# Kernel optimization log

Measured on AMD Instinct MI355X. Metric: run time of the kernel, lower is better.

The kernel has to match this reference:

```python
import jax, jax.numpy as jnp
import numpy as np
from jax import lax

D = 256          # embed_dims
NLP = 2          # NumLinePoints
B, H, W = 4, 64, 64
NQ = H * W       # 4096
NK = 4096
BN_EPS = 0.001


def setup_inputs() -> dict:
    key = jax.random.key(0)
    ks = jax.random.split(key, 16)
    inp = {
        "query": jax.random.normal(ks[0], (B, D, H, W), jnp.float32),
        "v": jax.random.normal(ks[1], (B, NK, D), jnp.float32),
        "query_pos": jax.random.normal(ks[2], (B, NQ, D), jnp.float32),
        "key_pos": jax.random.normal(ks[3], (B, NK, D), jnp.float32),
        "other_W": jax.random.uniform(ks[4], (B, NK), jnp.float32),
        # params (torch Linear convention: weight [out, in], y = x @ W.T + b)
        "w_vs": jax.random.normal(ks[5], (D, D), jnp.float32) * (1.0 / np.sqrt(D)),
        "mlp_w1": jax.random.normal(ks[6], (D, 2 * D), jnp.float32) * (1.0 / np.sqrt(2 * D)),
        "mlp_b1": jnp.zeros((D,), jnp.float32),
        "mlp_w2": jax.random.normal(ks[7], (D, D), jnp.float32) * (1.0 / np.sqrt(D)),
        "mlp_b2": jnp.zeros((D,), jnp.float32),
        "conv1_w": jax.random.normal(ks[8], (D, D, 3, 3), jnp.float32) * (1.0 / np.sqrt(9 * D)),
        "bn_gamma": jnp.ones((D,), jnp.float32),
        "bn_beta": jnp.zeros((D,), jnp.float32),
        "bn_mean": jnp.zeros((D,), jnp.float32),
        "bn_var": jnp.ones((D,), jnp.float32),
        "conv2_w": jax.random.normal(ks[9], (D, D, 1, 1), jnp.float32) * (1.0 / np.sqrt(D)),
        "conv2_b": jnp.zeros((D,), jnp.float32),
    }
    return inp


def _forward(query, v, query_pos, key_pos, other_W,
             w_vs, mlp_w1, mlp_b1, mlp_w2, mlp_b2,
             conv1_w, bn_gamma, bn_beta, bn_mean, bn_var,
             conv2_w, conv2_b):
    # v projection (no bias)
    v = jnp.einsum('bkd,ed->bke', v, w_vs)
    # ref_point_head: repeat query_pos along feature dim, then 2-layer MLP
    qp = jnp.concatenate([query_pos] * NLP, axis=-1)          # [B,NQ,2D]
    qp = jax.nn.relu(jnp.einsum('bqd,hd->bqh', qp, mlp_w1) + mlp_b1)
    qp = jnp.einsum('bqh,eh->bqe', qp, mlp_w2) + mlp_b2       # [B,NQ,D]
    # L2 normalize
    qn = qp / jnp.linalg.norm(qp, axis=-1, keepdims=True)
    kn = key_pos / jnp.linalg.norm(key_pos, axis=-1, keepdims=True)
    # similarity + ReLU + elementwise mask
    rel = jax.nn.relu(jnp.einsum('bqd,bkd->bqk', qn, kn))     # [B,NQ,NK]
    rel = rel * other_W[:, None, :]
    out = jnp.einsum('bqk,bkd->bqd', rel, v)                  # [B,NQ,D]
    # reshape to feature map [B,D,H,W]
    out = out.transpose(0, 2, 1).reshape(query.shape)
    # fuse: conv3x3 (no bias) + BN (eval) + SiLU, then conv1x1 (+bias)
    x = lax.conv_general_dilated(out, conv1_w, (1, 1), 'SAME',
                                 dimension_numbers=('NCHW', 'OIHW', 'NCHW'))
    inv = bn_gamma / jnp.sqrt(bn_var + BN_EPS)
    x = x * inv[None, :, None, None] + (bn_beta - bn_mean * inv)[None, :, None, None]
    x = x * jax.nn.sigmoid(x)  # SiLU
    x = lax.conv_general_dilated(x, conv2_w, (1, 1), 'SAME',
                                 dimension_numbers=('NCHW', 'OIHW', 'NCHW'))
    x = x + conv2_b[None, :, None, None]
    return query + x


def reference(query, v, query_pos, key_pos, other_W,
              w_vs, mlp_w1, mlp_b1, mlp_w2, mlp_b2,
              conv1_w, bn_gamma, bn_beta, bn_mean, bn_var,
              conv2_w, conv2_b):
    return _forward(query, v, query_pos, key_pos, other_W,
                    w_vs, mlp_w1, mlp_b1, mlp_w2, mlp_b2,
                    conv1_w, bn_gamma, bn_beta, bn_mean, bn_var,
                    conv2_w, conv2_b)
```

## Files before the change

kernel.cpp:

```cpp
#include <hip/hip_runtime.h>
#include <math.h>

constexpr int kB  = 4;
constexpr int kD  = 256;
constexpr int kNQ = 4096;
constexpr int kNK = 4096;
constexpr int kHW = 4096;

typedef __bf16 bf16x8 __attribute__((ext_vector_type(8)));
typedef float  f32x16 __attribute__((ext_vector_type(16)));

__device__ __forceinline__ unsigned short f2bf(float x) {
    unsigned int u = __builtin_bit_cast(unsigned int, x);
    u = (u + 0x7fffu + ((u >> 16) & 1u)) >> 16;
    return (unsigned short)u;
}

__global__ __launch_bounds__(256) void k_prep(
    const float* __restrict__ v_in, const float* __restrict__ ow, ushort* __restrict__ v_bf,
    const float* __restrict__ qpos, ushort* __restrict__ qpos_bf,
    const float* __restrict__ kpos, ushort* __restrict__ kn_bf,
    const float* __restrict__ conv1_w, ushort* __restrict__ w9p,
    const float* __restrict__ w_vs, ushort* __restrict__ wvs_bf,
    const float* __restrict__ mlp_w2, ushort* __restrict__ w2_bf,
    const float* __restrict__ conv2_w, ushort* __restrict__ c2_bf,
    const float* __restrict__ mlp_w1, ushort* __restrict__ w1e_bf)
{
    const int bid = blockIdx.x, t = threadIdx.x;
    if (bid < 4096) {
        const int i = bid * 256 + t;
        float4 v = ((const float4*)v_in)[i];
        const float wsc = ow[i >> 6];
        ushort4 o;
        o.x = f2bf(v.x * wsc); o.y = f2bf(v.y * wsc);
        o.z = f2bf(v.z * wsc); o.w = f2bf(v.w * wsc);
        ((ushort4*)v_bf)[i] = o;
    } else if (bid < 8192) {
        const int i = (bid - 4096) * 256 + t;
        float4 v = ((const float4*)qpos)[i];
        ushort4 o;
        o.x = f2bf(v.x); o.y = f2bf(v.y); o.z = f2bf(v.z); o.w = f2bf(v.w);
        ((ushort4*)qpos_bf)[i] = o;
    } else if (bid < 12288) {
        const int row  = (bid - 8192) * 4 + (t >> 6);
        const int lane = t & 63;
        float4 v = ((const float4*)(kpos + (size_t)row * 256))[lane];
        float ss = v.x * v.x + v.y * v.y + v.z * v.z + v.w * v.w;
        #pragma unroll
        for (int off = 32; off; off >>= 1) ss += __shfl_xor(ss, off, 64);
        const float rn = 1.0f / sqrtf(ss);
        ushort4 o;
        o.x = f2bf(v.x * rn); o.y = f2bf(v.y * rn);
        o.z = f2bf(v.z * rn); o.w = f2bf(v.w * rn);
        ((ushort4*)(kn_bf + (size_t)row * 256))[lane] = o;
    } else if (bid < 14592) {
        const int idx = bid - 12288;
        const int s = idx >> 8, co = idx & 255, ci = t;
        const int oidx = ((s * 8 + (co >> 5)) * 16 + (ci >> 4)) * 512
                       + ((ci >> 3) & 1) * 256 + (co & 31) * 8 + (ci & 7);
        w9p[oidx] = f2bf(conv1_w[((size_t)co * 256 + ci) * 9 + s]);
    } else if (bid < 14784) {
        const float* src = (bid < 14656) ? w_vs : (bid < 14720) ? mlp_w2 : conv2_w;
        ushort* dst = (bid < 14656) ? wvs_bf : (bid < 14720) ? w2_bf : c2_bf;
        const int i = ((bid - 14592) & 63) * 256 + t;
        float4 v = ((const float4*)src)[i];
        ushort4 o;
        o.x = f2bf(v.x); o.y = f2bf(v.y); o.z = f2bf(v.z); o.w = f2bf(v.w);
        ((ushort4*)dst)[i] = o;
    } else {
        const int h = bid - 14784;
        w1e_bf[h * 256 + t] = f2bf(mlp_w1[h * 512 + t] + mlp_w1[h * 512 + 256 + t]);
    }
}

template<int EPI, int RELU>
__global__ __launch_bounds__(256, 2) void k_gemm_mfma(
    const ushort* __restrict__ A, const ushort* __restrict__ W,
    const float* __restrict__ bias, void* __restrict__ outp)
{
    const int t = threadIdx.x, w = t >> 6, l = t & 63, lr = l & 31, lh = l >> 5;
    const int m0 = (blockIdx.x >> 2) * 128;
    const int n0 = (blockIdx.x & 3) * 64;
    const int wm = w >> 1, wn = w & 1;
    const ushort* Ar0 = A + (size_t)(m0 + wm * 64 + lr) * 256 + lh * 8;
    const ushort* Ar1 = Ar0 + 32 * 256;
    const ushort* Wr  = W + (size_t)(n0 + wn * 32 + lr) * 256 + lh * 8;
    f32x16 c0{}, c1{};
    #pragma unroll
    for (int ks = 0; ks < 16; ++ks) {
        bf16x8 a0 = *(const bf16x8*)(Ar0 + ks * 16);
        bf16x8 a1 = *(const bf16x8*)(Ar1 + ks * 16);
        bf16x8 wf = *(const bf16x8*)(Wr + ks * 16);
        c0 = __builtin_amdgcn_mfma_f32_32x32x16_bf16(a0, wf, c0, 0, 0, 0);
        c1 = __builtin_amdgcn_mfma_f32_32x32x16_bf16(a1, wf, c1, 0, 0, 0);
    }
    const int n = n0 + wn * 32 + lr;
    float bb = bias ? bias[n] : 0.f;
    if constexpr (EPI == 2) {
        __shared__ ushort tr[64][136];
        #pragma unroll
        for (int r = 0; r < 16; ++r) {
            const int ml = wm * 64 + (r & 3) + 8 * (r >> 2) + 4 * lh;
            float v0 = c0[r], v1 = c1[r];
            if (RELU) { v0 = fmaxf(v0, 0.f); v1 = fmaxf(v1, 0.f); }
            tr[wn * 32 + lr][ml]      = f2bf(v0);
            tr[wn * 32 + lr][ml + 32] = f2bf(v1);
        }
        __syncthreads();
        ushort* out = (ushort*)outp;
        const int b = m0 >> 12, mm = m0 & 4095;
        const int row = t >> 2, seg = t & 3;
        uint4 u0 = *(uint4*)&tr[row][seg * 32];
        uint4 u1 = *(uint4*)&tr[row][seg * 32 + 8];
        uint4 u2 = *(uint4*)&tr[row][seg * 32 + 16];
        uint4 u3 = *(uint4*)&tr[row][seg * 32 + 24];
        ushort* ob = out + ((size_t)(b * 128 + (mm >> 5) + seg) * 256 + n0 + row) * 32;
        *(uint4*)ob        = u0; *(uint4*)(ob + 8)  = u1;
        *(uint4*)(ob + 16) = u2; *(uint4*)(ob + 24) = u3;
    } else {
        #pragma unroll
        for (int r = 0; r < 16; ++r) {
            const int m = m0 + wm * 64 + (r & 3) + 8 * (r >> 2) + 4 * lh;
            float v0 = c0[r] + bb, v1 = c1[r] + bb;
            if (RELU) { v0 = fmaxf(v0, 0.f); v1 = fmaxf(v1, 0.f); }
            if constexpr (EPI == 0) {
                float* out = (float*)outp;
                out[(size_t)m * 256 + n]      = v0;
                out[(size_t)(m + 32) * 256 + n] = v1;
            } else {
                ushort* out = (ushort*)outp;
                out[(size_t)m * 256 + n]      = f2bf(v0);
                out[(size_t)(m + 32) * 256 + n] = f2bf(v1);
            }
        }
    }
}

__global__ __launch_bounds__(256) void k_l2norm_bf16(const float* __restrict__ in,
                                                     ushort* __restrict__ out) {
    const int row  = blockIdx.x * 4 + (threadIdx.x >> 6);
    const int lane = threadIdx.x & 63;
    float4 v = ((const float4*)(in + (size_t)row * 256))[lane];
    float ss = v.x * v.x + v.y * v.y + v.z * v.z + v.w * v.w;
    #pragma unroll
    for (int off = 32; off; off >>= 1) ss += __shfl_xor(ss, off, 64);
    const float rn = 1.0f / sqrtf(ss);
    ushort4 o;
    o.x = f2bf(v.x * rn); o.y = f2bf(v.y * rn);
    o.z = f2bf(v.z * rn); o.w = f2bf(v.w * rn);
    ((ushort4*)(out + (size_t)row * 256))[lane] = o;
}

__global__ __launch_bounds__(512, 2) void k_attn_mfma(
    const ushort* __restrict__ qn, const ushort* __restrict__ kn,
    const ushort* __restrict__ vpT, ushort* __restrict__ X)
{
    __shared__ __align__(16) char lds[147456];
    const int t = threadIdx.x, w = t >> 6, l = t & 63, lr = l & 31, lh = l >> 5;
    const int dh = w >> 2, qg = (w >> 1) & 1, kh = w & 1;
    const int bid0 = blockIdx.x;
    const int L = (bid0 & 7) * 32 + (bid0 >> 3);
    const int b = L >> 6, qt = L & 63;
    const int q0 = qt << 6;
    union U4 { unsigned u[4]; bf16x8 v; };

    int koff[4], voff[4];
    #pragma unroll
    for (int i = 0; i < 4; ++i) {
        const int p = i * 512 + t;
        {
            const int R = p >> 5, sl = p & 31;
            koff[i] = R * 512 + ((sl ^ (R & 31)) << 4);
        }
        {
            const int sub = p >> 10, q = p & 1023;
            const int R = q >> 4, ch = (q & 15) ^ (R & 15);
            voff[i] = sub * 16384 + ((ch >> 2) * 64 + R) * 64 + ((ch & 3) << 4);
        }
    }
    const char* kgb = (const char*)(kn + (size_t)b * 4096 * 256);
    const char* vgb = (const char*)vpT + (size_t)b * 128 * 16384;

    #define STAGE_K(bb, tc) do { \
        const char* ks_ = kgb + (size_t)(tc) * 32768; \
        char* kd_ = lds + (bb) * 32768; \
        _Pragma("unroll") \
        for (int i_ = 0; i_ < 4; ++i_) \
            __builtin_amdgcn_global_load_lds( \
                (const __attribute__((address_space(1))) unsigned*)(ks_ + koff[i_]), \
                (__attribute__((address_space(3))) unsigned*)(kd_ + (i_ * 512 + w * 64) * 16), 16, 0, 0); \
        } while (0)
    #define STAGE_V(bb, tc) do { \
        const char* vs_ = vgb + (size_t)(tc) * 32768; \
        char* vd_ = lds + 65536 + (bb) * 32768; \
        _Pragma("unroll") \
        for (int i_ = 0; i_ < 4; ++i_) \
            __builtin_amdgcn_global_load_lds( \
                (const __attribute__((address_space(1))) unsigned*)(vs_ + voff[i_]), \
                (__attribute__((address_space(3))) unsigned*)(vd_ + (i_ * 512 + w * 64) * 16), 16, 0, 0); \
        } while (0)

    const ushort* qrow = qn + ((size_t)b * 4096 + q0 + qg * 32 + lr) * 256 + lh * 8;
    bf16x8 qf[16];
    #pragma unroll
    for (int ks = 0; ks < 16; ++ks) qf[ks] = *(const bf16x8*)(qrow + ks * 16);

    f32x16 oa0{}, oa1{}, oa2{}, oa3{};
    bf16x8 pf0{}, pf1{};

    STAGE_K(0, 0);
    __syncthreads();
    for (int tt = 0; tt <= 64; ++tt) {
        if (tt < 64) {
            if (tt + 1 < 64) STAGE_K((tt + 1) & 1, tt + 1);
            STAGE_V(tt & 1, tt);
        }
        if (tt > 0) {
            const char* vb = lds + 65536 + ((tt - 1) & 1) * 32768 + kh * 16384;
            bf16x8 qp0, qp1;
            if (dh == 0) { qp0 = pf0; qp1 = pf1; }
            else {
                const unsigned* pr = (const unsigned*)(lds + 131072
                                   + ((tt - 1) & 1) * 8192 + (qg * 2 + kh) * 2048);
                U4 a0, a1;
                #pragma unroll
                for (int wd = 0; wd < 4; ++wd) {
                    a0.u[wd] = pr[wd * 64 + l];
                    a1.u[wd] = pr[(4 + wd) * 64 + l];
                }
                qp0 = a0.v; qp1 = a1.v;
            }
            #define PVD(OA, DB) { \
                const int R_  = (((DB) & 1)) * 32 + lr; \
                const int sg_ = dh * 2 + ((DB) >> 1); \
                bf16x8 v0_ = *(const bf16x8*)(vb + R_ * 256 + ((((sg_ << 2) + lh)     ^ (lr & 15)) << 4)); \
                bf16x8 v1_ = *(const bf16x8*)(vb + R_ * 256 + ((((sg_ << 2) + 2 + lh) ^ (lr & 15)) << 4)); \
                OA = __builtin_amdgcn_mfma_f32_32x32x16_bf16(v0_, qp0, OA, 0, 0, 0); \
                OA = __builtin_amdgcn_mfma_f32_32x32x16_bf16(v1_, qp1, OA, 0, 0, 0); }
            PVD(oa0, 0) PVD(oa1, 1) PVD(oa2, 2) PVD(oa3, 3)
            #undef PVD
        }
        if (dh == 0 && tt < 64) {
            const char* kb = lds + (tt & 1) * 32768 + kh * 16384;
            f32x16 s0{}, s1{}, s2{}, s3{};
            #pragma unroll
            for (int ks = 0; ks < 16; ks += 4) {
                bf16x8 k0 = *(const bf16x8*)(kb + lr * 512 + (((2 * ks     + lh) ^ lr) << 4));
                bf16x8 k1 = *(const bf16x8*)(kb + lr * 512 + (((2 * ks + 2 + lh) ^ lr) << 4));
                bf16x8 k2 = *(const bf16x8*)(kb + lr * 512 + (((2 * ks + 4 + lh) ^ lr) << 4));
                bf16x8 k3 = *(const bf16x8*)(kb + lr * 512 + (((2 * ks + 6 + lh) ^ lr) << 4));
                s0 = __builtin_amdgcn_mfma_f32_32x32x16_bf16(k0, qf[ks],     s0, 0, 0, 0);
                s1 = __builtin_amdgcn_mfma_f32_32x32x16_bf16(k1, qf[ks + 1], s1, 0, 0, 0);
                s2 = __builtin_amdgcn_mfma_f32_32x32x16_bf16(k2, qf[ks + 2], s2, 0, 0, 0);
                s3 = __builtin_amdgcn_mfma_f32_32x32x16_bf16(k3, qf[ks + 3], s3, 0, 0, 0);
            }
            f32x16 s = (s0 + s1) + (s2 + s3);
            #define PKR(A, B) ((unsigned)f2bf(fmaxf((A), 0.f)) | ((unsigned)f2bf(fmaxf((B), 0.f)) << 16))
            unsigned p01 = PKR(s[0],  s[1]),  p23 = PKR(s[2],  s[3]);
            unsigned p45 = PKR(s[4],  s[5]),  p67 = PKR(s[6],  s[7]);
            unsigned p89 = PKR(s[8],  s[9]),  pAB = PKR(s[10], s[11]);
            unsigned pCD = PKR(s[12], s[13]), pEF = PKR(s[14], s[15]);
            #undef PKR
            unsigned e1a = lh ? p01 : p45,  e2a = lh ? p23 : p67;
            unsigned e1b = lh ? p89 : pCD,  e2b = lh ? pAB : pEF;
            unsigned f1a = (unsigned)__shfl_xor((int)e1a, 32, 64);
            unsigned f2a = (unsigned)__shfl_xor((int)e2a, 32, 64);
            unsigned f1b = (unsigned)__shfl_xor((int)e1b, 32, 64);
            unsigned f2b = (unsigned)__shfl_xor((int)e2b, 32, 64);
            U4 a0, a1;
            a0.u[0] = lh ? f1a : p01;  a0.u[1] = lh ? f2a : p23;
            a0.u[2] = lh ? p45 : f1a;  a0.u[3] = lh ? p67 : f2a;
            a1.u[0] = lh ? f1b : p89;  a1.u[1] = lh ? f2b : pAB;
            a1.u[2] = lh ? pCD : f1b;  a1.u[3] = lh ? pEF : f2b;
            pf0 = a0.v; pf1 = a1.v;
            unsigned* pw = (unsigned*)(lds + 131072 + (tt & 1) * 8192 + (qg * 2 + kh) * 2048);
            #pragma unroll
            for (int wd = 0; wd < 4; ++wd) {
                pw[wd * 64 + l]       = a0.u[wd];
                pw[(4 + wd) * 64 + l] = a1.u[wd];
            }
        }
        if (tt < 64) __syncthreads();
    }
    #undef STAGE_K
    #undef STAGE_V
    float* red = (float*)lds;
    const int rowbase = ((qg * 2 + dh) * 32 + lr) * 132;
    if (kh == 1) {
        #define REDW(OA, DB) _Pragma("unroll") \
            for (int r = 0; r < 16; r += 2) { \
                const int d_ = (DB) * 32 + (r & 3) + 8 * (r >> 2) + 4 * lh; \
                *(float2*)&red[rowbase + d_] = make_float2((OA)[r], (OA)[r + 1]); }
        REDW(oa0, 0) REDW(oa1, 1) REDW(oa2, 2) REDW(oa3, 3)
        #undef REDW
    }
    __syncthreads();
    if (kh == 0) {
        ushort* Xb = X + ((size_t)b * 4096 + q0 + qg * 32 + lr) * 256 + dh * 128;
        #define OUTD(OA, DB) _Pragma("unroll") \
            for (int r = 0; r < 16; r += 2) { \
                const int d_ = (DB) * 32 + (r & 3) + 8 * (r >> 2) + 4 * lh; \
                float2 p = *(float2*)&red[rowbase + d_]; \
                ushort2 u_; u_.x = f2bf((OA)[r] + p.x); u_.y = f2bf((OA)[r + 1] + p.y); \
                *(ushort2*)(Xb + d_) = u_; }
        OUTD(oa0, 0) OUTD(oa1, 1) OUTD(oa2, 2) OUTD(oa3, 3)
        #undef OUTD
    }
}

__global__ __launch_bounds__(256, 2) void k_conv3_mfma(
    const ushort* __restrict__ X, const ushort* __restrict__ w9p,
    const float* __restrict__ bn_g, const float* __restrict__ bn_b,
    const float* __restrict__ bn_m, const float* __restrict__ bn_v,
    ushort* __restrict__ Y)
{
    __shared__ __align__(16) char smem[67584];
    float* bnv = (float*)(smem + 65536);
    const int t = threadIdx.x, w = t >> 6, l = t & 63, lr = l & 31, lh = l >> 5;
    {
        float inv = bn_g[t] * rsqrtf(bn_v[t] + 1e-3f);
        bnv[t]       = inv;
        bnv[256 + t] = bn_b[t] - bn_m[t] * inv;
    }
    const int bid = blockIdx.x;
    const int b = bid >> 7, ct = (bid >> 5) & 3, pt = bid & 31;
    const int co0 = ct * 64, p0 = pt * 128;
    const int wc = w >> 1, wp = w & 1;
    const int h0 = pt * 2 + wp;
    const int cb = ct * 2 + wc;
    const char* Xbytes = (const char*)(X + (size_t)b * 4096 * 256);
    const bf16x8 bz = {};
    f32x16 o0{}, o1{};

    #define CSTAGE(bufb, st_) do { \
        const char* src_ = Xbytes + (ptrdiff_t)(p0 + 64 * ((st_) >> 1) - 64) * 512 \
                         + ((st_) & 1) * 256; \
        char* dst_ = smem + (bufb) * 32768; \
        _Pragma("unroll") \
        for (int i_ = 0; i_ < 8; ++i_) { \
            const int di_ = i_ * 256 + t; \
            const int R_ = di_ >> 4, sl_ = di_ & 15; \
            __builtin_amdgcn_global_load_lds( \
                (const __attribute__((address_space(1))) unsigned*)(src_ + (ptrdiff_t)R_ * 512 + ((sl_ ^ (R_ & 15)) << 4)), \
                (__attribute__((address_space(3))) unsigned*)(dst_ + di_ * 16), 16, 0, 0); \
        } } while (0)

    CSTAGE(0, 0);
    __syncthreads();
    for (int st = 0; st < 6; ++st) {
        if (st < 5) CSTAGE((st + 1) & 1, st + 1);
        if (st < 5) asm volatile("s_waitcnt vmcnt(8)" ::: "memory");
        else        asm volatile("s_waitcnt vmcnt(0)" ::: "memory");
        __builtin_amdgcn_s_barrier();
        const char* xb = smem + (st & 1) * 32768;
        const int dyi = st >> 1, cih = st & 1;
        const int hh = h0 + dyi - 1;
        if (hh >= 0 && hh <= 63) {
            __builtin_amdgcn_s_setprio(1);
            #pragma unroll
            for (int dxi = 0; dxi < 3; ++dxi) {
                const int dx = dxi - 1;
                const int s = dyi * 3 + dxi;
                const bool mA = (dxi == 0) && (lr == 0);
                const bool mB = (dxi == 2) && (lr == 31);
                const int R0 = mA ? 0 : (wp * 64 + lr + dx);
                const int R1 = mB ? 0 : (wp * 64 + lr + dx + 32);
                const ushort* wb = w9p + ((size_t)(s * 8 + cb) * 16 + cih * 8) * 512 + l * 8;
                #pragma unroll
                for (int k8 = 0; k8 < 8; ++k8) {
                    bf16x8 af = *(const bf16x8*)(wb + k8 * 512);
                    bf16x8 b0 = *(const bf16x8*)(xb + R0 * 256 + (((k8 * 2 + lh) ^ (R0 & 15)) << 4));
                    bf16x8 b1 = *(const bf16x8*)(xb + R1 * 256 + (((k8 * 2 + lh) ^ (R1 & 15)) << 4));
                    if (mA) b0 = bz;
                    if (mB) b1 = bz;
                    o0 = __builtin_amdgcn_mfma_f32_32x32x16_bf16(af, b0, o0, 0, 0, 0);
                    o1 = __builtin_amdgcn_mfma_f32_32x32x16_bf16(af, b1, o1, 0, 0, 0);
                }
            }
            __builtin_amdgcn_s_setprio(0);
        }
        __builtin_amdgcn_s_barrier();
    }
    #undef CSTAGE
    ushort (*tr)[72] = (ushort(*)[72])smem;
    #pragma unroll
    for (int r = 0; r < 16; ++r) {
        const int co_l = wc * 32 + (r & 3) + 8 * (r >> 2) + 4 * lh;
        const int co = co0 + co_l;
        const float inv = bnv[co], add = bnv[256 + co];
        float x0 = o0[r] * inv + add;
        float x1 = o1[r] * inv + add;
        x0 = x0 / (1.f + expf(-x0));
        x1 = x1 / (1.f + expf(-x1));
        tr[wp * 64 + lr][co_l]      = f2bf(x0);
        tr[wp * 64 + 32 + lr][co_l] = f2bf(x1);
    }
    __syncthreads();
    const int pp = t >> 1, half = t & 1;
    uint4 u0 = *(uint4*)&tr[pp][half * 32];
    uint4 u1 = *(uint4*)&tr[pp][half * 32 + 8];
    uint4 u2 = *(uint4*)&tr[pp][half * 32 + 16];
    uint4 u3 = *(uint4*)&tr[pp][half * 32 + 24];
    ushort* yb = Y + ((size_t)b * 4096 + p0 + pp) * 256 + co0 + half * 32;
    *(uint4*)yb        = u0; *(uint4*)(yb + 8)  = u1;
    *(uint4*)(yb + 16) = u2; *(uint4*)(yb + 24) = u3;
}

__global__ __launch_bounds__(256, 2) void k_conv1x1_mfma(
    const ushort* __restrict__ Y, const ushort* __restrict__ W2,
    const float* __restrict__ bias2, const float* __restrict__ query,
    float* __restrict__ out)
{
    const int t = threadIdx.x, w = t >> 6, l = t & 63, lr = l & 31, lh = l >> 5;
    const int bid = blockIdx.x;
    const int b = bid >> 7, ct = (bid >> 5) & 3, pt = bid & 31;
    const int co0 = ct * 64, p0 = pt * 128;
    const int wc = w >> 1, wp = w & 1;
    const ushort* Wr = W2 + (size_t)(co0 + wc * 32 + lr) * 256 + lh * 8;
    const ushort* Yp = Y + ((size_t)b * 4096 + p0 + wp * 64 + lr) * 256 + lh * 8;
    f32x16 o0{}, o1{};
    #pragma unroll
    for (int ks = 0; ks < 16; ++ks) {
        bf16x8 wf = *(const bf16x8*)(Wr + ks * 16);
        bf16x8 y0 = *(const bf16x8*)(Yp + ks * 16);
        bf16x8 y1 = *(const bf16x8*)(Yp + 32 * 256 + ks * 16);
        o0 = __builtin_amdgcn_mfma_f32_32x32x16_bf16(wf, y0, o0, 0, 0, 0);
        o1 = __builtin_amdgcn_mfma_f32_32x32x16_bf16(wf, y1, o1, 0, 0, 0);
    }
    #pragma unroll
    for (int r = 0; r < 16; ++r) {
        const int co = co0 + wc * 32 + (r & 3) + 8 * (r >> 2) + 4 * lh;
        const float bb = bias2[co];
        const size_t base = ((size_t)b * 256 + co) * 4096 + p0 + wp * 64 + lr;
        out[base]      = o0[r] + bb + query[base];
        out[base + 32] = o1[r] + bb + query[base + 32];
    }
}

extern "C" void kernel_launch(void* const* d_in, const int* in_sizes, int n_in,
                              void* d_out, int out_size, void* d_ws, size_t ws_size,
                              hipStream_t stream) {
    const float* query   = (const float*)d_in[0];
    const float* v_in    = (const float*)d_in[1];
    const float* qpos    = (const float*)d_in[2];
    const float* kpos    = (const float*)d_in[3];
    const float* otherW  = (const float*)d_in[4];
    const float* w_vs    = (const float*)d_in[5];
    const float* mlp_w1  = (const float*)d_in[6];
    const float* mlp_b1  = (const float*)d_in[7];
    const float* mlp_w2  = (const float*)d_in[8];
    const float* mlp_b2  = (const float*)d_in[9];
    const float* conv1_w = (const float*)d_in[10];
    const float* bn_g    = (const float*)d_in[11];
    const float* bn_b    = (const float*)d_in[12];
    const float* bn_m    = (const float*)d_in[13];
    const float* bn_v    = (const float*)d_in[14];
    const float* conv2_w = (const float*)d_in[15];
    const float* conv2_b = (const float*)d_in[16];
    float* out = (float*)d_out;
    char* base = (char*)d_ws;

    constexpr size_t MB = 1u << 20;
    ushort* v_bf    = (ushort*)(base);
    ushort* qpos_bf = (ushort*)(base + 8 * MB);
    float*  qp_f32  = (float*) (base);
    ushort* qhid_bf = (ushort*)(base + 16 * MB);
    ushort* X_bf    = (ushort*)(base + 16 * MB);
    ushort* qn_bf   = (ushort*)(base + 24 * MB);
    ushort* Y_bf    = (ushort*)(base + 24 * MB);
    ushort* kn_bf   = (ushort*)(base + 32 * MB);
    ushort* vT_bf   = (ushort*)(base + 40 * MB);
    ushort* wvs_bf  = (ushort*)(base + 48 * MB);
    ushort* w1e_bf  = (ushort*)(base + 48 * MB + 128 * 1024);
    ushort* w2_bf   = (ushort*)(base + 48 * MB + 256 * 1024);
    ushort* c2_bf   = (ushort*)(base + 48 * MB + 384 * 1024);
    ushort* w9p_bf  = (ushort*)(base + 48 * MB + 512 * 1024);

    k_prep<<<15040, 256, 0, stream>>>(v_in, otherW, v_bf, qpos, qpos_bf,
                                      kpos, kn_bf, conv1_w, w9p_bf,
                                      w_vs, wvs_bf, mlp_w2, w2_bf,
                                      conv2_w, c2_bf, mlp_w1, w1e_bf);
    k_gemm_mfma<2, 0><<<512, 256, 0, stream>>>(v_bf, wvs_bf, nullptr, vT_bf);
    k_gemm_mfma<1, 1><<<512, 256, 0, stream>>>(qpos_bf, w1e_bf, mlp_b1, qhid_bf);
    k_gemm_mfma<0, 0><<<512, 256, 0, stream>>>(qhid_bf, w2_bf, mlp_b2, qp_f32);
    k_l2norm_bf16<<<4096, 256, 0, stream>>>(qp_f32, qn_bf);
    k_attn_mfma<<<256, 512, 0, stream>>>(qn_bf, kn_bf, vT_bf, X_bf);
    k_conv3_mfma<<<512, 256, 0, stream>>>(X_bf, w9p_bf, bn_g, bn_b, bn_m, bn_v, Y_bf);
    k_conv1x1_mfma<<<512, 256, 0, stream>>>(Y_bf, c2_bf, conv2_b, query, out);
}
```

Baseline: 209.4 us.

## Stage GEMM and 1x1-conv tiles in swizzled LDS with 128x128 blocks

The projection/MLP GEMMs and the final 1x1 conv move from 128x64 tiles, where each wave read its operands straight from global memory, to 128x128 tiles per 512-thread block. Both operand tiles are first copied into 128KB of LDS with direct global-to-LDS loads, using an XOR swizzle so the MFMA fragment reads avoid bank conflicts. This is meant to cut redundant global traffic, since operands are now shared across eight waves. In exchange it allows one block per CU, halves the grid, and has no overlap between the bulk load and compute.

```diff
diff --git a/kernel.cpp b/kernel.cpp
--- a/kernel.cpp
+++ b/kernel.cpp
@@ -74,30 +74,49 @@
 }
 
 template<int EPI, int RELU>
-__global__ __launch_bounds__(256, 2) void k_gemm_mfma(
+__global__ __launch_bounds__(512, 1) void k_gemm_mfma(
     const ushort* __restrict__ A, const ushort* __restrict__ W,
     const float* __restrict__ bias, void* __restrict__ outp)
 {
+    __shared__ __align__(16) char lds[131072];
     const int t = threadIdx.x, w = t >> 6, l = t & 63, lr = l & 31, lh = l >> 5;
-    const int m0 = (blockIdx.x >> 2) * 128;
-    const int n0 = (blockIdx.x & 3) * 64;
-    const int wm = w >> 1, wn = w & 1;
-    const ushort* Ar0 = A + (size_t)(m0 + wm * 64 + lr) * 256 + lh * 8;
-    const ushort* Ar1 = Ar0 + 32 * 256;
-    const ushort* Wr  = W + (size_t)(n0 + wn * 32 + lr) * 256 + lh * 8;
+    const int wm = w >> 2, wn = w & 3;
+    const int m0 = (blockIdx.x >> 1) * 128;
+    const int n0 = (blockIdx.x & 1) * 128;
+    const char* Ab = (const char*)A + (size_t)m0 * 512;
+    const char* Wb = (const char*)W + (size_t)n0 * 512;
+    #pragma unroll
+    for (int i = 0; i < 8; ++i) {
+        const int p = i * 512 + t;
+        const int R = p >> 5, sl = p & 31;
+        const int so = R * 512 + ((sl ^ (R & 31)) << 4);
+        __builtin_amdgcn_global_load_lds(
+            (const __attribute__((address_space(1))) unsigned*)(Ab + so),
+            (__attribute__((address_space(3))) unsigned*)(lds + p * 16), 16, 0, 0);
+        __builtin_amdgcn_global_load_lds(
+            (const __attribute__((address_space(1))) unsigned*)(Wb + so),
+            (__attribute__((address_space(3))) unsigned*)(lds + 65536 + p * 16), 16, 0, 0);
+    }
+    __syncthreads();
+    const char* Abuf = lds;
+    const char* Wbuf = lds + 65536;
+    const int ar0 = wm * 64 + lr, ar1 = ar0 + 32;
+    const int wrr = wn * 32 + lr;
     f32x16 c0{}, c1{};
     #pragma unroll
     for (int ks = 0; ks < 16; ++ks) {
-        bf16x8 a0 = *(const bf16x8*)(Ar0 + ks * 16);
-        bf16x8 a1 = *(const bf16x8*)(Ar1 + ks * 16);
-        bf16x8 wf = *(const bf16x8*)(Wr + ks * 16);
+        const int j = 2 * ks + lh;
+        bf16x8 a0 = *(const bf16x8*)(Abuf + ar0 * 512 + ((j ^ lr) << 4));
+        bf16x8 a1 = *(const bf16x8*)(Abuf + ar1 * 512 + ((j ^ lr) << 4));
+        bf16x8 wf = *(const bf16x8*)(Wbuf + wrr * 512 + ((j ^ lr) << 4));
         c0 = __builtin_amdgcn_mfma_f32_32x32x16_bf16(a0, wf, c0, 0, 0, 0);
         c1 = __builtin_amdgcn_mfma_f32_32x32x16_bf16(a1, wf, c1, 0, 0, 0);
     }
     const int n = n0 + wn * 32 + lr;
     float bb = bias ? bias[n] : 0.f;
     if constexpr (EPI == 2) {
-        __shared__ ushort tr[64][136];
+        __syncthreads();
+        ushort (*tr)[136] = (ushort(*)[136])lds;
         #pragma unroll
         for (int r = 0; r < 16; ++r) {
             const int ml = wm * 64 + (r & 3) + 8 * (r >> 2) + 4 * lh;
@@ -406,34 +425,56 @@
     *(uint4*)(yb + 16) = u2; *(uint4*)(yb + 24) = u3;
 }
 
-__global__ __launch_bounds__(256, 2) void k_conv1x1_mfma(
+__global__ __launch_bounds__(512, 1) void k_conv1x1_mfma(
     const ushort* __restrict__ Y, const ushort* __restrict__ W2,
     const float* __restrict__ bias2, const float* __restrict__ query,
     float* __restrict__ out)
 {
+    __shared__ __align__(16) char lds[131072];
     const int t = threadIdx.x, w = t >> 6, l = t & 63, lr = l & 31, lh = l >> 5;
+    const int wc = w >> 2, wp = w & 3;
     const int bid = blockIdx.x;
-    const int b = bid >> 7, ct = (bid >> 5) & 3, pt = bid & 31;
-    const int co0 = ct * 64, p0 = pt * 128;
-    const int wc = w >> 1, wp = w & 1;
-    const ushort* Wr = W2 + (size_t)(co0 + wc * 32 + lr) * 256 + lh * 8;
-    const ushort* Yp = Y + ((size_t)b * 4096 + p0 + wp * 64 + lr) * 256 + lh * 8;
+    const int b = bid >> 6, pt = (bid >> 1) & 31, ct = bid & 1;
+    const int p0 = pt * 128, co0 = ct * 128;
+    const char* Yb = (const char*)Y + ((size_t)b * 4096 + p0) * 512;
+    const char* Wb = (const char*)W2 + (size_t)co0 * 512;
+    #pragma unroll
+    for (int i = 0; i < 8; ++i) {
+        const int p = i * 512 + t;
+        const int R = p >> 5, sl = p & 31;
+        const int so = R * 512 + ((sl ^ (R & 31)) << 4);
+        __builtin_amdgcn_global_load_lds(
+            (const __attribute__((address_space(1))) unsigned*)(Yb + so),
+            (__attribute__((address_space(3))) unsigned*)(lds + p * 16), 16, 0, 0);
+        __builtin_amdgcn_global_load_lds(
+            (const __attribute__((address_space(1))) unsigned*)(Wb + so),
+            (__attribute__((address_space(3))) unsigned*)(lds + 65536 + p * 16), 16, 0, 0);
+    }
+    __syncthreads();
+    const char* Ybuf = lds;
+    const char* Wbuf = lds + 65536;
+    const int cr0 = wc * 64 + lr, cr1 = cr0 + 32;
+    const int yr  = wp * 32 + lr;
     f32x16 o0{}, o1{};
     #pragma unroll
     for (int ks = 0; ks < 16; ++ks) {
-        bf16x8 wf = *(const bf16x8*)(Wr + ks * 16);
-        bf16x8 y0 = *(const bf16x8*)(Yp + ks * 16);
-        bf16x8 y1 = *(const bf16x8*)(Yp + 32 * 256 + ks * 16);
-        o0 = __builtin_amdgcn_mfma_f32_32x32x16_bf16(wf, y0, o0, 0, 0, 0);
-        o1 = __builtin_amdgcn_mfma_f32_32x32x16_bf16(wf, y1, o1, 0, 0, 0);
-    }
+        const int j = 2 * ks + lh;
+        bf16x8 w0 = *(const bf16x8*)(Wbuf + cr0 * 512 + ((j ^ lr) << 4));
+        bf16x8 w1 = *(const bf16x8*)(Wbuf + cr1 * 512 + ((j ^ lr) << 4));
+        bf16x8 yf = *(const bf16x8*)(Ybuf + yr  * 512 + ((j ^ lr) << 4));
+        o0 = __builtin_amdgcn_mfma_f32_32x32x16_bf16(w0, yf, o0, 0, 0, 0);
+        o1 = __builtin_amdgcn_mfma_f32_32x32x16_bf16(w1, yf, o1, 0, 0, 0);
+    }
+    const int p = p0 + wp * 32 + lr;
     #pragma unroll
     for (int r = 0; r < 16; ++r) {
-        const int co = co0 + wc * 32 + (r & 3) + 8 * (r >> 2) + 4 * lh;
-        const float bb = bias2[co];
-        const size_t base = ((size_t)b * 256 + co) * 4096 + p0 + wp * 64 + lr;
-        out[base]      = o0[r] + bb + query[base];
-        out[base + 32] = o1[r] + bb + query[base + 32];
+        const int crow = (r & 3) + 8 * (r >> 2) + 4 * lh;
+        const int coA = co0 + wc * 64 + crow;
+        const int coB = coA + 32;
+        const size_t baseA = ((size_t)b * 256 + coA) * 4096 + p;
+        const size_t baseB = ((size_t)b * 256 + coB) * 4096 + p;
+        out[baseA] = o0[r] + bias2[coA] + query[baseA];
+        out[baseB] = o1[r] + bias2[coB] + query[baseB];
     }
 }
 
@@ -480,11 +521,11 @@
                                       kpos, kn_bf, conv1_w, w9p_bf,
                                       w_vs, wvs_bf, mlp_w2, w2_bf,
                                       conv2_w, c2_bf, mlp_w1, w1e_bf);
-    k_gemm_mfma<2, 0><<<512, 256, 0, stream>>>(v_bf, wvs_bf, nullptr, vT_bf);
-    k_gemm_mfma<1, 1><<<512, 256, 0, stream>>>(qpos_bf, w1e_bf, mlp_b1, qhid_bf);
-    k_gemm_mfma<0, 0><<<512, 256, 0, stream>>>(qhid_bf, w2_bf, mlp_b2, qp_f32);
+    k_gemm_mfma<2, 0><<<256, 512, 0, stream>>>(v_bf, wvs_bf, nullptr, vT_bf);
+    k_gemm_mfma<1, 1><<<256, 512, 0, stream>>>(qpos_bf, w1e_bf, mlp_b1, qhid_bf);
+    k_gemm_mfma<0, 0><<<256, 512, 0, stream>>>(qhid_bf, w2_bf, mlp_b2, qp_f32);
     k_l2norm_bf16<<<4096, 256, 0, stream>>>(qp_f32, qn_bf);
     k_attn_mfma<<<256, 512, 0, stream>>>(qn_bf, kn_bf, vT_bf, X_bf);
     k_conv3_mfma<<<512, 256, 0, stream>>>(X_bf, w9p_bf, bn_g, bn_b, bn_m, bn_v, Y_bf);
-    k_conv1x1_mfma<<<512, 256, 0, stream>>>(Y_bf, c2_bf, conv2_b, query, out);
-}
+    k_conv1x1_mfma<<<256, 512, 0, stream>>>(Y_bf, c2_bf, conv2_b, query, out);
+}
```

Result: faster. 183.7 us (-12.3%).
